# Kernel tuning notes

Measured on AMD Instinct MI355X. Metric: run time of the kernel, lower is better.

Reference implementation:

```python
import jax, jax.numpy as jnp
import numpy as np

B, N, DIM, H = 2, 4096, 512, 8
DH = DIM // H  # head dim = 64


def setup_inputs() -> dict:
    key = jax.random.key(0)
    kx, kw, kb = jax.random.split(key, 3)
    x = jax.random.normal(kx, (B, N, DIM), dtype=jnp.float32)
    W = jax.random.normal(kw, (DIM, 3 * DIM), dtype=jnp.float32) / np.sqrt(DIM)
    b = jax.random.normal(kb, (3 * DIM,), dtype=jnp.float32) * 0.02
    return {"x": x, "W": W, "b": b}


def reference(x, W, b):
    Bx, n, d = x.shape
    qvk = x @ W + b  # [B, n, 3*dim]
    # torch.chunk order in source: q, v, k
    q, v, k = jnp.split(qvk, 3, axis=-1)

    def heads(t):  # [B, n, dim] -> [B, h, n, dh]
        return t.reshape(Bx, n, H, DH).transpose(0, 2, 1, 3)

    q, v, k = heads(q), heads(v), heads(k)
    # full (non-fused) attention: materializes [B, h, n, n] scores
    scale = jnp.einsum('bhqd,bhkd->bhqk', q, k) / jnp.sqrt(jnp.float32(DH))
    atn = jax.nn.softmax(scale, axis=-1)
    out = jnp.einsum('bhqk,bhkd->bhqd', atn, v)  # [B, h, n, dh]
    # concat_head: [B, h, n, dh] -> [B, n, h*dh]
    out = out.transpose(0, 2, 1, 3).reshape(Bx, n, H * DH)
    return out
```

## Files before the change

kernel.cpp:

```cpp
#include <hip/hip_runtime.h>
#include <hip/hip_bf16.h>
#include <math.h>

#define BB    2
#define NN    4096
#define DIM   512
#define NH    8
#define DH    64
#define NC    1536
#define MM    (BB*NN)

typedef __bf16 bf16x8 __attribute__((ext_vector_type(8)));
typedef __bf16 bf16x4 __attribute__((ext_vector_type(4)));
typedef float  f32x4  __attribute__((ext_vector_type(4)));

#define QSCALE 0.18033688011112042f

__device__ __forceinline__ int swz(int c) { return c ^ (((c >> 3) ^ (c >> 6)) & 7); }
__device__ __forceinline__ int kswz(int g) { return g ^ ((g >> 3) & 3) ^ (((g >> 6) & 1) << 2); }

__device__ __forceinline__ void gl_lds16(const __hip_bfloat16* g, __bf16* l) {
    __builtin_amdgcn_global_load_lds(
        (const __attribute__((address_space(1))) unsigned int*)g,
        (__attribute__((address_space(3))) unsigned int*)l, 16, 0, 0);
}

__device__ __forceinline__ int sniff(const unsigned short* x) {
    unsigned short v = x[2 * (threadIdx.x & 63)];
    int e = (v >> 7) & 0xFF;
    unsigned long long m = __ballot(e >= 110 && e <= 140);
    return __popcll(m) >= 48;
}

__device__ __forceinline__ f32x4 mfma32(bf16x8 a, bf16x8 b, f32x4 c) {
    return __builtin_amdgcn_mfma_f32_16x16x32_bf16(a, b, c, 0, 0, 0);
}

__global__ __launch_bounds__(256) void prep_kernel(
    const void* __restrict__ xin, const void* __restrict__ win,
    const void* __restrict__ bin,
    __hip_bfloat16* __restrict__ Xb, __hip_bfloat16* __restrict__ WT,
    float* __restrict__ Bf)
{
    __shared__ __bf16 tile[64][68];
    int bfmode = sniff((const unsigned short*)xin);
    int bid = blockIdx.x;
    int t = threadIdx.x;
    if (bid < 2048) {
        if (bfmode) return;
        int i = (bid * 256 + t) * 8;
        const float* xf = (const float*)xin + i;
        bf16x8 v;
        for (int j = 0; j < 8; j++) v[j] = (__bf16)xf[j];
        *(bf16x8*)(Xb + i) = v;
    } else if (bid < 2048 + 192) {
        int tl = bid - 2048;
        int kt = tl / 24, nt = tl % 24;
        int tx = t & 63, tyq = t >> 6;
        for (int r = 0; r < 16; r++) {
            int kl = r * 4 + tyq;
            int gi = (kt * 64 + kl) * NC + nt * 64 + tx;
            float v = bfmode ? __bfloat162float(((const __hip_bfloat16*)win)[gi])
                             : ((const float*)win)[gi];
            tile[kl][tx] = (__bf16)v;
        }
        __syncthreads();
        for (int r = 0; r < 16; r++) {
            int nl = r * 4 + tyq;
            WT[(size_t)(nt * 64 + nl) * DIM + kt * 64 + tx] = (__hip_bfloat16)(float)tile[tx][nl];
        }
    } else {
        int i = (bid - 2048 - 192) * 256 + t;
        if (i < NC)
            Bf[i] = bfmode ? __bfloat162float(((const __hip_bfloat16*)bin)[i])
                           : ((const float*)bin)[i];
    }
}

__global__ __launch_bounds__(256, 3) void qkv_gemm(
    const unsigned short* __restrict__ xs,
    const __hip_bfloat16* __restrict__ Xb,
    const __hip_bfloat16* __restrict__ WT,
    const float* __restrict__ Bf,
    __hip_bfloat16* __restrict__ Qb,
    __hip_bfloat16* __restrict__ Kb,
    __hip_bfloat16* __restrict__ Vt)
{
    __shared__ __align__(16) __bf16 smem[16384];
    __bf16* Xs = smem;
    __bf16* Ws = smem + 8192;

    int bfmode = sniff(xs);
    const __hip_bfloat16* X = bfmode ? (const __hip_bfloat16*)xs : Xb;

    int wave = threadIdx.x >> 6, lane = threadIdx.x & 63;
    int lane16 = lane & 15, quad = lane >> 4;
    int bm = blockIdx.x / 12, bn = blockIdx.x % 12;
    int m0b = bm * 128, n0b = bn * 128;
    int wm = wave >> 1, wn = wave & 1;
    int m0 = m0b + wm * 64, n0 = n0b + wn * 64;

    int xgo[2], sbase[2];
    for (int j = 0; j < 2; j++) {
        int p = (wave * 2 + j) * 64 + lane;
        int g = swz(p);
        xgo[j] = (g >> 2) * DIM + (g & 3) * 8;
        sbase[j] = (wave * 2 + j) * 512;
    }
    int aoff[4], boff[4];
    for (int mi = 0; mi < 4; mi++)
        aoff[mi] = swz((wm * 64 + mi * 16 + lane16) * 4 + quad) * 8;
    for (int ni = 0; ni < 4; ni++)
        boff[ni] = swz((wn * 64 + ni * 16 + lane16) * 4 + quad) * 8;

    const __hip_bfloat16* Xg = X  + (size_t)m0b * DIM;
    const __hip_bfloat16* Wg = WT + (size_t)n0b * DIM;

    for (int j = 0; j < 2; j++) {
        gl_lds16(Xg + xgo[j], &Xs[sbase[j]]);
        gl_lds16(Wg + xgo[j], &Ws[sbase[j]]);
    }
    __syncthreads();

    f32x4 acc[4][4] = {};
    for (int k0 = 0; k0 < DIM; k0 += 32) {
        int cur = (k0 >> 5) & 1, nbuf = cur ^ 1;
        int k1 = (k0 + 32) & (DIM - 1);
        for (int j = 0; j < 2; j++) {
            gl_lds16(Xg + k1 + xgo[j], &Xs[nbuf * 4096 + sbase[j]]);
            gl_lds16(Wg + k1 + xgo[j], &Ws[nbuf * 4096 + sbase[j]]);
        }
        bf16x8 a[4], b[4];
        for (int mi = 0; mi < 4; mi++) a[mi] = *(const bf16x8*)&Xs[cur * 4096 + aoff[mi]];
        for (int ni = 0; ni < 4; ni++) b[ni] = *(const bf16x8*)&Ws[cur * 4096 + boff[ni]];
        for (int mi = 0; mi < 4; mi++)
            for (int ni = 0; ni < 4; ni++)
                acc[mi][ni] = mfma32(a[mi], b[ni], acc[mi][ni]);
        __syncthreads();
    }
    __bf16* epi = smem + wave * 4096;

    int sec = n0b >> 9;
    int bidx = m0b >> 12;
    if (sec == 1) {
        for (int ni = 0; ni < 4; ni++) {
            int nloc = ni * 16 + lane16;
            float bv = Bf[n0 + nloc];
            for (int mi = 0; mi < 4; mi++) {
                bf16x4 pk;
                for (int r = 0; r < 4; r++) pk[r] = (__bf16)(acc[mi][ni][r] + bv);
                int idx = swz(nloc * 8 + mi * 2 + (quad >> 1)) * 8 + (quad & 1) * 4;
                *(bf16x4*)&epi[idx] = pk;
            }
        }
        int hl = (n0 - 512) >> 6;
        int mbase = m0b - bidx * NN + wm * 64;
        for (int p = 0; p < 8; p++) {
            int n = p * 8 + (lane >> 3), mc = lane & 7;
            bf16x8 vv = *(const bf16x8*)&epi[swz(n * 8 + mc) * 8];
            *(bf16x8*)(Vt + ((size_t)(bidx * 8 + hl) * 64 + n) * NN + mbase + mc * 8) = vv;
        }
    } else {
        bool isQ = (sec == 0);
        int h = (n0 & 511) >> 6;
        for (int mi = 0; mi < 4; mi++) {
            for (int ni = 0; ni < 4; ni++) {
                float bv = Bf[n0 + ni * 16 + lane16];
                int dl = ni * 16 + lane16;
                for (int r = 0; r < 4; r++) {
                    int row = mi * 16 + quad * 4 + r;
                    float v = acc[mi][ni][r] + bv;
                    if (isQ) v *= QSCALE;
                    epi[swz(row * 8 + (dl >> 3)) * 8 + (dl & 7)] = (__bf16)v;
                }
            }
        }
        __hip_bfloat16* dst = isQ ? Qb : Kb;
        int bh = bidx * 8 + h;
        int mbase = m0 - bidx * NN;
        for (int p = 0; p < 8; p++) {
            int row = p * 8 + (lane >> 3), dc = lane & 7;
            bf16x8 vv = *(const bf16x8*)&epi[swz(row * 8 + dc) * 8];
            *(bf16x8*)(dst + ((size_t)bh * NN + mbase + row) * DH + dc * 8) = vv;
        }
    }
}

__global__ __launch_bounds__(128, 4) void attn_partial(
    const __hip_bfloat16* __restrict__ Qb,
    const __hip_bfloat16* __restrict__ Kb,
    const __hip_bfloat16* __restrict__ Vt,
    float* __restrict__ Op,
    float* __restrict__ Lp)
{
    __shared__ __align__(16) __bf16 Kst[2][2048];
    __shared__ __align__(16) __bf16 Vst[2][2048];

    int wave = threadIdx.x >> 6, lane = threadIdx.x & 63;
    int lane16 = lane & 15, quad = lane >> 4;

    int orig = blockIdx.x;
    int nbid = (orig & 7) * 256 + (orig >> 3);
    int bh = nbid >> 7;
    int qt = (nbid >> 1) & 63;
    int kh = nbid & 1;
    int q0 = qt * 64 + wave * 32;
    int khbase = kh * 2048, kend = khbase + 2048;

    const __hip_bfloat16* Qh = Qb + (size_t)bh * NN * DH;
    const __hip_bfloat16* Kh = Kb + (size_t)bh * NN * DH;
    const __hip_bfloat16* Vh = Vt + (size_t)bh * DH * NN;

    bf16x8 bq[2][2];
    #pragma unroll
    for (int qf = 0; qf < 2; qf++)
        #pragma unroll
        for (int kc = 0; kc < 2; kc++)
            bq[qf][kc] = *(const bf16x8*)(Qh + (size_t)(q0 + qf * 16 + lane16) * DH + kc * 32 + quad * 8);

    int kgo[2], vgo[2], sbase[2];
    #pragma unroll
    for (int j = 0; j < 2; j++) {
        int p = (wave * 2 + j) * 64 + lane;
        int gk = kswz(p);
        kgo[j] = (gk >> 3) * DH + (gk & 7) * 8;
        int gv = swz(p);
        vgo[j] = (gv >> 2) * NN + (gv & 3) * 8;
        sbase[j] = (wave * 2 + j) * 512;
    }
    int koff[2][2];
    #pragma unroll
    for (int kf = 0; kf < 2; kf++) {
        int key = (lane16 >> 2) * 8 + 4 * kf + (lane16 & 3);
        #pragma unroll
        for (int kc = 0; kc < 2; kc++)
            koff[kf][kc] = kswz(key * 8 + kc * 4 + quad) * 8;
    }
    int voff[4];
    #pragma unroll
    for (int dt = 0; dt < 4; dt++)
        voff[dt] = swz((dt * 16 + lane16) * 4 + quad) * 8;

    for (int j = 0; j < 2; j++) {
        gl_lds16(Kh + (size_t)khbase * DH + kgo[j], &Kst[0][sbase[j]]);
        gl_lds16(Vh + khbase + vgo[j], &Vst[0][sbase[j]]);
    }
    __syncthreads();

    bf16x8 ones8;
    #pragma unroll
    for (int j = 0; j < 8; j++) ones8[j] = (__bf16)1.0f;
    f32x4 o[4][2] = {};
    f32x4 ol[2] = {};

    for (int k0 = khbase; k0 < kend; k0 += 32) {
        int cur = ((k0 - khbase) >> 5) & 1, nb = cur ^ 1;
        int k1 = (k0 + 32 < kend) ? (k0 + 32) : khbase;
        for (int j = 0; j < 2; j++) {
            gl_lds16(Kh + (size_t)k1 * DH + kgo[j], &Kst[nb][sbase[j]]);
            gl_lds16(Vh + k1 + vgo[j], &Vst[nb][sbase[j]]);
        }

        bf16x8 ka[2][2];
        #pragma unroll
        for (int kf = 0; kf < 2; kf++)
            #pragma unroll
            for (int kc = 0; kc < 2; kc++)
                ka[kf][kc] = *(const bf16x8*)&Kst[cur][koff[kf][kc]];
        f32x4 s[2][2];
        #pragma unroll
        for (int kf = 0; kf < 2; kf++)
            #pragma unroll
            for (int qf = 0; qf < 2; qf++) {
                f32x4 t = {};
                t = mfma32(ka[kf][0], bq[qf][0], t);
                t = mfma32(ka[kf][1], bq[qf][1], t);
                s[kf][qf] = t;
            }

        bf16x4 pt[2][2];
        #pragma unroll
        for (int kf = 0; kf < 2; kf++)
            #pragma unroll
            for (int qf = 0; qf < 2; qf++)
                #pragma unroll
                for (int r = 0; r < 4; r++)
                    pt[kf][qf][r] = (__bf16)__builtin_amdgcn_exp2f(s[kf][qf][r]);

        bf16x8 av[4];
        #pragma unroll
        for (int dt = 0; dt < 4; dt++)
            av[dt] = *(const bf16x8*)&Vst[cur][voff[dt]];
        #pragma unroll
        for (int qf = 0; qf < 2; qf++) {
            bf16x8 pb = __builtin_shufflevector(pt[0][qf], pt[1][qf],
                                                0, 1, 2, 3, 4, 5, 6, 7);
            #pragma unroll
            for (int dt = 0; dt < 4; dt++)
                o[dt][qf] = mfma32(av[dt], pb, o[dt][qf]);
            ol[qf] = mfma32(ones8, pb, ol[qf]);
        }

        __syncthreads();
    }

    float* Ob = Op + ((size_t)kh * 16 + bh) * NN * DH;
    #pragma unroll
    for (int qf = 0; qf < 2; qf++)
        #pragma unroll
        for (int dt = 0; dt < 4; dt++)
            *(f32x4*)(Ob + (size_t)(q0 + qf * 16 + lane16) * DH + dt * 16 + quad * 4) = o[dt][qf];
    if (quad == 0) {
        #pragma unroll
        for (int qf = 0; qf < 2; qf++)
            Lp[((size_t)kh * 16 + bh) * NN + q0 + qf * 16 + lane16] = ol[qf][0];
    }
}

__global__ __launch_bounds__(256) void reduce_kernel(
    const float* __restrict__ Op, const float* __restrict__ Lp,
    void* __restrict__ OutV, const unsigned short* __restrict__ xs)
{
    int bfmode = sniff(xs);
    int i = blockIdx.x * 256 + threadIdx.x;
    size_t e = (size_t)i * 4;
    int c = (int)(e & 511);
    size_t bq = e >> 9;
    int h = c >> 6, d = c & 63;
    int b = (int)(bq >> 12);
    int q = (int)(bq & 4095);
    size_t bh = (size_t)b * 8 + h;
    size_t oa = (bh * NN + q) * DH + d;
    f32x4 v0 = *(const f32x4*)(Op + oa);
    f32x4 v1 = *(const f32x4*)(Op + (size_t)16 * NN * DH + oa);
    float l = Lp[bh * NN + q] + Lp[(size_t)16 * NN + bh * NN + q];
    float rinv = 1.0f / l;
    f32x4 r;
    #pragma unroll
    for (int j = 0; j < 4; j++) r[j] = (v0[j] + v1[j]) * rinv;
    if (bfmode) {
        bf16x4 pk;
        #pragma unroll
        for (int j = 0; j < 4; j++) pk[j] = (__bf16)r[j];
        *(bf16x4*)((__hip_bfloat16*)OutV + e) = pk;
    } else {
        *(f32x4*)((float*)OutV + e) = r;
    }
}

extern "C" void kernel_launch(void* const* d_in, const int* in_sizes, int n_in,
                              void* d_out, int out_size, void* d_ws, size_t ws_size,
                              hipStream_t stream) {
    char* ws = (char*)d_ws;
    __hip_bfloat16* Qb = (__hip_bfloat16*)ws;
    __hip_bfloat16* Kb = Qb + (size_t)BB * NH * NN * DH;
    __hip_bfloat16* Vt = Kb + (size_t)BB * NH * NN * DH;
    __hip_bfloat16* WT = Vt + (size_t)BB * NH * NN * DH;
    __hip_bfloat16* Xb = WT + (size_t)NC * DIM;
    float* Bf = (float*)(Xb + (size_t)MM * DIM);
    float* Op = (float*)WT;
    float* Lp = Op + (size_t)2 * 16 * NN * DH;

    prep_kernel<<<2048 + 192 + 6, 256, 0, stream>>>(d_in[0], d_in[1], d_in[2], Xb, WT, Bf);
    qkv_gemm<<<(MM / 128) * (NC / 128), 256, 0, stream>>>(
        (const unsigned short*)d_in[0], Xb, WT, Bf, Qb, Kb, Vt);
    attn_partial<<<2048, 128, 0, stream>>>(Qb, Kb, Vt, Op, Lp);
    reduce_kernel<<<4096, 256, 0, stream>>>(Op, Lp, d_out, (const unsigned short*)d_in[0]);
}
```

Measured before the change: 189.7 us.

## Fuse split-K attention halves and reduction into one block-level kernel

Replaces the two-kernel split-K attention (each block handles one key half, writing fp32 partial outputs and row sums to global memory, followed by a reduce kernel) with a single kernel. There, 4 waves per block process both key halves for the same query tile and combine them through shared memory. The normalized result is written directly to the output in the concat-head layout via an LDS-staged epilogue. This removes the fp32 partial round-trip through HBM and one kernel launch. In exchange, block count halves, LDS per block grows to 32KB, and an extra block-level sync plus a serialized epilogue run on half the waves.

```diff
diff --git a/kernel.cpp b/kernel.cpp
--- a/kernel.cpp
+++ b/kernel.cpp
@@ -186,26 +186,29 @@
     }
 }
 
-__global__ __launch_bounds__(128, 4) void attn_partial(
+__global__ __launch_bounds__(256, 4) void attn_fused(
     const __hip_bfloat16* __restrict__ Qb,
     const __hip_bfloat16* __restrict__ Kb,
     const __hip_bfloat16* __restrict__ Vt,
-    float* __restrict__ Op,
-    float* __restrict__ Lp)
+    void* __restrict__ OutV,
+    const unsigned short* __restrict__ xs)
 {
-    __shared__ __align__(16) __bf16 Kst[2][2048];
-    __shared__ __align__(16) __bf16 Vst[2][2048];
-
+    __shared__ __align__(16) __bf16 smem[16384];
+
+    int bfmode = sniff(xs);
     int wave = threadIdx.x >> 6, lane = threadIdx.x & 63;
     int lane16 = lane & 15, quad = lane >> 4;
+    int half = wave >> 1, qw = wave & 1;
 
     int orig = blockIdx.x;
-    int nbid = (orig & 7) * 256 + (orig >> 3);
-    int bh = nbid >> 7;
-    int qt = (nbid >> 1) & 63;
-    int kh = nbid & 1;
-    int q0 = qt * 64 + wave * 32;
-    int khbase = kh * 2048, kend = khbase + 2048;
+    int nbid = (orig & 7) * 128 + (orig >> 3);
+    int bh = nbid >> 6;
+    int qt = nbid & 63;
+    int q0 = qt * 64 + qw * 32;
+    int khbase = half * 2048;
+
+    __bf16* Kst = smem + half * 8192;
+    __bf16* Vst = smem + half * 8192 + 4096;
 
     const __hip_bfloat16* Qh = Qb + (size_t)bh * NN * DH;
     const __hip_bfloat16* Kh = Kb + (size_t)bh * NN * DH;
@@ -221,12 +224,12 @@
     int kgo[2], vgo[2], sbase[2];
     #pragma unroll
     for (int j = 0; j < 2; j++) {
-        int p = (wave * 2 + j) * 64 + lane;
+        int p = (qw * 2 + j) * 64 + lane;
         int gk = kswz(p);
         kgo[j] = (gk >> 3) * DH + (gk & 7) * 8;
         int gv = swz(p);
         vgo[j] = (gv >> 2) * NN + (gv & 3) * 8;
-        sbase[j] = (wave * 2 + j) * 512;
+        sbase[j] = (qw * 2 + j) * 512;
     }
     int koff[2][2];
     #pragma unroll
@@ -242,8 +245,8 @@
         voff[dt] = swz((dt * 16 + lane16) * 4 + quad) * 8;
 
     for (int j = 0; j < 2; j++) {
-        gl_lds16(Kh + (size_t)khbase * DH + kgo[j], &Kst[0][sbase[j]]);
-        gl_lds16(Vh + khbase + vgo[j], &Vst[0][sbase[j]]);
+        gl_lds16(Kh + (size_t)khbase * DH + kgo[j], &Kst[sbase[j]]);
+        gl_lds16(Vh + khbase + vgo[j], &Vst[sbase[j]]);
     }
     __syncthreads();
 
@@ -253,12 +256,12 @@
     f32x4 o[4][2] = {};
     f32x4 ol[2] = {};
 
-    for (int k0 = khbase; k0 < kend; k0 += 32) {
-        int cur = ((k0 - khbase) >> 5) & 1, nb = cur ^ 1;
-        int k1 = (k0 + 32 < kend) ? (k0 + 32) : khbase;
+    for (int it = 0; it < 64; ++it) {
+        int cur = it & 1, nb = cur ^ 1;
+        int k1 = khbase + ((it + 1) & 63) * 32;
         for (int j = 0; j < 2; j++) {
-            gl_lds16(Kh + (size_t)k1 * DH + kgo[j], &Kst[nb][sbase[j]]);
-            gl_lds16(Vh + k1 + vgo[j], &Vst[nb][sbase[j]]);
+            gl_lds16(Kh + (size_t)k1 * DH + kgo[j], &Kst[nb * 2048 + sbase[j]]);
+            gl_lds16(Vh + k1 + vgo[j], &Vst[nb * 2048 + sbase[j]]);
         }
 
         bf16x8 ka[2][2];
@@ -266,7 +269,7 @@
         for (int kf = 0; kf < 2; kf++)
             #pragma unroll
             for (int kc = 0; kc < 2; kc++)
-                ka[kf][kc] = *(const bf16x8*)&Kst[cur][koff[kf][kc]];
+                ka[kf][kc] = *(const bf16x8*)&Kst[cur * 2048 + koff[kf][kc]];
         f32x4 s[2][2];
         #pragma unroll
         for (int kf = 0; kf < 2; kf++)
@@ -290,7 +293,7 @@
         bf16x8 av[4];
         #pragma unroll
         for (int dt = 0; dt < 4; dt++)
-            av[dt] = *(const bf16x8*)&Vst[cur][voff[dt]];
+            av[dt] = *(const bf16x8*)&Vst[cur * 2048 + voff[dt]];
         #pragma unroll
         for (int qf = 0; qf < 2; qf++) {
             bf16x8 pb = __builtin_shufflevector(pt[0][qf], pt[1][qf],
@@ -304,47 +307,50 @@
         __syncthreads();
     }
 
-    float* Ob = Op + ((size_t)kh * 16 + bh) * NN * DH;
-    #pragma unroll
-    for (int qf = 0; qf < 2; qf++)
-        #pragma unroll
-        for (int dt = 0; dt < 4; dt++)
-            *(f32x4*)(Ob + (size_t)(q0 + qf * 16 + lane16) * DH + dt * 16 + quad * 4) = o[dt][qf];
-    if (quad == 0) {
-        #pragma unroll
-        for (int qf = 0; qf < 2; qf++)
-            Lp[((size_t)kh * 16 + bh) * NN + q0 + qf * 16 + lane16] = ol[qf][0];
-    }
-}
-
-__global__ __launch_bounds__(256) void reduce_kernel(
-    const float* __restrict__ Op, const float* __restrict__ Lp,
-    void* __restrict__ OutV, const unsigned short* __restrict__ xs)
-{
-    int bfmode = sniff(xs);
-    int i = blockIdx.x * 256 + threadIdx.x;
-    size_t e = (size_t)i * 4;
-    int c = (int)(e & 511);
-    size_t bq = e >> 9;
-    int h = c >> 6, d = c & 63;
-    int b = (int)(bq >> 12);
-    int q = (int)(bq & 4095);
-    size_t bh = (size_t)b * 8 + h;
-    size_t oa = (bh * NN + q) * DH + d;
-    f32x4 v0 = *(const f32x4*)(Op + oa);
-    f32x4 v1 = *(const f32x4*)(Op + (size_t)16 * NN * DH + oa);
-    float l = Lp[bh * NN + q] + Lp[(size_t)16 * NN + bh * NN + q];
-    float rinv = 1.0f / l;
-    f32x4 r;
-    #pragma unroll
-    for (int j = 0; j < 4; j++) r[j] = (v0[j] + v1[j]) * rinv;
-    if (bfmode) {
-        bf16x4 pk;
-        #pragma unroll
-        for (int j = 0; j < 4; j++) pk[j] = (__bf16)r[j];
-        *(bf16x4*)((__hip_bfloat16*)OutV + e) = pk;
-    } else {
-        *(f32x4*)((float*)OutV + e) = r;
+    float* Osh = (float*)smem;
+    float* lsh = Osh + 2 * 32 * 68;
+    if (half == 1) {
+        #pragma unroll
+        for (int qf = 0; qf < 2; qf++) {
+            #pragma unroll
+            for (int dt = 0; dt < 4; dt++)
+                *(f32x4*)&Osh[(qw * 32 + qf * 16 + lane16) * 68 + dt * 16 + quad * 4] = o[dt][qf];
+            if (quad == 0) lsh[qw * 32 + qf * 16 + lane16] = ol[qf][0];
+        }
+    }
+    __syncthreads();
+    if (half == 0) {
+        __bf16* epi = smem + 8832 + qw * 2048;
+        #pragma unroll
+        for (int qf = 0; qf < 2; qf++) {
+            float l = ol[qf][0] + lsh[qw * 32 + qf * 16 + lane16];
+            float rinv = 1.0f / l;
+            #pragma unroll
+            for (int dt = 0; dt < 4; dt++) {
+                f32x4 po = *(const f32x4*)&Osh[(qw * 32 + qf * 16 + lane16) * 68 + dt * 16 + quad * 4];
+                #pragma unroll
+                for (int r = 0; r < 4; r++) {
+                    int d = dt * 16 + quad * 4 + r;
+                    int row = qf * 16 + lane16;
+                    epi[swz(row * 8 + (d >> 3)) * 8 + (d & 7)] = (__bf16)((o[dt][qf][r] + po[r]) * rinv);
+                }
+            }
+        }
+        int bidx = bh >> 3, h = bh & 7;
+        for (int p = 0; p < 4; p++) {
+            int row = p * 8 + (lane >> 3), mc = lane & 7;
+            bf16x8 vv = *(const bf16x8*)&epi[swz(row * 8 + mc) * 8];
+            size_t base = ((size_t)bidx * NN + q0 + row) * DIM + h * 64 + mc * 8;
+            if (bfmode) {
+                *(bf16x8*)((__hip_bfloat16*)OutV + base) = vv;
+            } else {
+                float* op = (float*)OutV + base;
+                f32x4 f0, f1;
+                for (int j = 0; j < 4; j++) { f0[j] = (float)vv[j]; f1[j] = (float)vv[4 + j]; }
+                *(f32x4*)op = f0;
+                *(f32x4*)(op + 4) = f1;
+            }
+        }
     }
 }
 
@@ -358,12 +364,9 @@
     __hip_bfloat16* WT = Vt + (size_t)BB * NH * NN * DH;
     __hip_bfloat16* Xb = WT + (size_t)NC * DIM;
     float* Bf = (float*)(Xb + (size_t)MM * DIM);
-    float* Op = (float*)WT;
-    float* Lp = Op + (size_t)2 * 16 * NN * DH;
 
     prep_kernel<<<2048 + 192 + 6, 256, 0, stream>>>(d_in[0], d_in[1], d_in[2], Xb, WT, Bf);
     qkv_gemm<<<(MM / 128) * (NC / 128), 256, 0, stream>>>(
         (const unsigned short*)d_in[0], Xb, WT, Bf, Qb, Kb, Vt);
-    attn_partial<<<2048, 128, 0, stream>>>(Qb, Kb, Vt, Op, Lp);
-    reduce_kernel<<<4096, 256, 0, stream>>>(Op, Lp, d_out, (const unsigned short*)d_in[0]);
-}
+    attn_fused<<<1024, 256, 0, stream>>>(Qb, Kb, Vt, d_out, (const unsigned short*)d_in[0]);
+}
```

After: 182.3 us. 3.9% less time.
